# Optimization experiments

Measured on AMD Instinct MI355X. Metric: run time of the kernel, lower is better.

The kernel has to match this reference:

```python
import jax, jax.numpy as jnp
import numpy as np

ALPHA = 0.2  # LeakyReLU negative slope
NEG_BIG = jnp.float32(-9e15)


def _leaky_relu(x):
    return jnp.where(x > 0, x, ALPHA * x)


def gat_layer(h, adj, w, a):
    """One GATLayer with concat=True (ELU output), dropout=0 (eval mode).
    h: [N, F_in], adj: [N, N] int, w: [F_in, F_out], a: [2*F_out, 1].
    """
    Wh = h @ w                         # [N, F_out]
    f_out = w.shape[1]
    Wh1 = Wh @ a[:f_out]               # [N, 1]
    Wh2 = Wh @ a[f_out:]               # [N, 1]
    e = _leaky_relu(Wh1 + Wh2.T)       # [N, N] dense additive scores
    att = jnp.where(adj > 0, e, NEG_BIG)
    att = jax.nn.softmax(att, axis=1)  # row softmax
    return jax.nn.elu(att @ Wh)        # [N, F_out]


def setup_inputs() -> dict:
    N, F_IN, H, NHEADS = 4096, 128, 64, 4
    key = jax.random.key(0)
    ks = jax.random.split(key, 9)
    s = jnp.float32(0.1)  # keep logits in a sane range
    x = jax.random.normal(ks[0], (N, F_IN), jnp.float32)
    adj = jax.random.randint(ks[1], (N, N), 0, 2, jnp.int32)
    return {
        "x": x,
        "adj": adj,
        "w_heads": jax.random.normal(ks[2], (NHEADS, F_IN, H), jnp.float32) * s,
        "a_heads": jax.random.normal(ks[3], (NHEADS, 2 * H, 1), jnp.float32) * s,
        "w_out": jax.random.normal(ks[4], (NHEADS * H, H), jnp.float32) * s,
        "a_out": jax.random.normal(ks[5], (2 * H, 1), jnp.float32) * s,
        "lin_w": jax.random.normal(ks[6], (H, F_IN), jnp.float32) * s,
        "lin_b": jnp.zeros((H,), jnp.float32),
        "outlin_w": jax.random.normal(ks[7], (H, H), jnp.float32) * s,
        "outlin_b": jnp.zeros((H,), jnp.float32),
    }


def reference(x, adj, w_heads, a_heads, w_out, a_out, lin_w, lin_b, outlin_w, outlin_b):
    N = x.shape[0]
    x_residual = x @ lin_w.T + lin_b                      # nn.Linear(input, hidden)
    # multi-head GAT layers, concatenated along features
    heads = jax.vmap(gat_layer, in_axes=(None, None, 0, 0))(x, adj, w_heads, a_heads)  # [nh, N, H]
    hcat = jnp.transpose(heads, (1, 0, 2)).reshape(N, -1)  # [N, nh*H]
    out = gat_layer(hcat, adj, w_out, a_out)               # out_att (concat=True => ELU)
    out = (x_residual + out) @ outlin_w.T + outlin_b       # out_linear
    return jax.nn.elu(out)
```

## Files before the change

kernel.cpp:

```cpp
#include <hip/hip_runtime.h>
#include <hip/hip_bf16.h>
#include <stdint.h>

#define F_IN 128
#define H 64
#define NH 4
#define KCH_H 16
#define KCH_O 32
#define LOG2E 1.44269504088896f

typedef __attribute__((ext_vector_type(8))) short bf16x8;
typedef __attribute__((ext_vector_type(4))) float floatx4;

static __device__ __forceinline__ unsigned short f2bf(float v) {
    __hip_bfloat16 b = __float2bfloat16(v);
    return *(unsigned short*)&b;
}
static __device__ __forceinline__ float bf2f(unsigned short u) {
    return __uint_as_float((unsigned int)u << 16);
}

__global__ void prep_kernel(const int* __restrict__ adj,
                            unsigned char* __restrict__ adjp,
                            const float* __restrict__ x,
                            const float* __restrict__ w_heads,
                            const float* __restrict__ a_heads,
                            const float* __restrict__ lin_w,
                            const float* __restrict__ lin_b,
                            unsigned short* __restrict__ Bpk,
                            float* __restrict__ x_res,
                            float* __restrict__ s1h,
                            float* __restrict__ s2h, int N) {
    const int bid = blockIdx.x;
    const int tid = threadIdx.x;
    const int KT = N >> 5;
    const int WH_BLOCKS = N / 8;

    if (bid >= WH_BLOCKS) {
        int idx = bid - WH_BLOCKS;
        int it = idx >> 3, rem = idx & 7, half = rem >> 2, zz = rem & 3;
        int i0 = it * 16;
        int n = tid & 15, q = (tid >> 4) & 3, w = tid >> 6;
        const int* row = adj + (size_t)(i0 + n) * N;
        unsigned char* dst = adjp + (size_t)it * KT * 64;
        int ktbase = half * (KT / 2) + zz * 16 + w;
#pragma unroll
        for (int j = 0; j < 4; ++j) {
            int kt = ktbase + 4 * j;
            int c0 = kt * 32 + q * 8;
            int4 a = *(const int4*)(row + c0);
            int4 b = *(const int4*)(row + c0 + 4);
            unsigned byte =
                (unsigned)(a.x > 0) | ((unsigned)(a.y > 0) << 1) |
                ((unsigned)(a.z > 0) << 2) | ((unsigned)(a.w > 0) << 3) |
                ((unsigned)(b.x > 0) << 4) | ((unsigned)(b.y > 0) << 5) |
                ((unsigned)(b.z > 0) << 6) | ((unsigned)(b.w > 0) << 7);
            dst[kt * 64 + q * 16 + n] = (unsigned char)byte;
        }
        return;
    }

    int h = tid >> 6, f = tid & 63;
    int i0 = bid * 8;
    __shared__ float xs[8][F_IN];
    __shared__ float lwT[F_IN][65];
    for (int e = tid; e < 8 * F_IN; e += 256)
        xs[e >> 7][e & 127] = x[(size_t)(i0 + (e >> 7)) * F_IN + (e & 127)];
    for (int e = tid; e < 64 * F_IN; e += 256) {
        int ff = e >> 7, k = e & 127;
        lwT[k][ff] = lin_w[e];
    }
    __syncthreads();
    float acc[8];
#pragma unroll
    for (int r = 0; r < 8; ++r) acc[r] = 0.f;
    float xr0 = 0.f, xr1 = 0.f;
    const float* w = w_heads + (size_t)h * F_IN * H + f;
#pragma unroll 4
    for (int k = 0; k < F_IN; ++k) {
        float wv = w[(size_t)k * H];
#pragma unroll
        for (int r = 0; r < 8; ++r) acc[r] += xs[r][k] * wv;
        float wx = lwT[k][f];
        xr0 += xs[h][k] * wx;
        xr1 += xs[h + 4][k] * wx;
    }
    {
        int kt = i0 >> 5, qq = (i0 >> 3) & 3;
        union { unsigned short s[8]; uint4 v; } t;
#pragma unroll
        for (int r = 0; r < 8; ++r) t.s[r] = f2bf(acc[r]);
        unsigned short* d = Bpk +
            (((size_t)(h * KT + kt) * 4 + (f >> 4)) * 64 + qq * 16 + (f & 15)) * 8;
        *(uint4*)d = t.v;
    }
    float b = lin_b[f];
    x_res[(size_t)(i0 + h) * H + f] = xr0 + b;
    x_res[(size_t)(i0 + h + 4) * H + f] = xr1 + b;
    float a1v = a_heads[(size_t)h * 2 * H + f];
    float a2v = a_heads[(size_t)h * 2 * H + H + f];
#pragma unroll
    for (int r = 0; r < 8; ++r) {
        float t1 = acc[r] * a1v;
        float t2 = acc[r] * a2v;
#pragma unroll
        for (int off = 32; off > 0; off >>= 1) {
            t1 += __shfl_xor(t1, off, 64);
            t2 += __shfl_xor(t2, off, 64);
        }
        if (f == 0) {
            s1h[(size_t)h * N + i0 + r] = t1 * LOG2E;
            s2h[(size_t)h * N + i0 + r] = t2 * LOG2E;
        }
    }
}

template <int KTC>
__global__ __launch_bounds__(256, 8)
void pv2_kernel(const unsigned char* __restrict__ adjp,
                const unsigned short* __restrict__ Bpk,
                const float* __restrict__ s1a,
                const float* __restrict__ s2a,
                unsigned short* __restrict__ outp, float* __restrict__ lp,
                int out_stride, int N) {
    const int h = blockIdx.y, z = blockIdx.z;
    const int KT = N >> 5;
    const int kt0 = z * KTC;
    const int tid = threadIdx.x;
    const int wave = tid >> 6, lane = tid & 63;
    const int n = lane & 15, q = lane >> 4;
    const int i0w = (blockIdx.x * 4 + wave) * 16;

    __shared__ float s2s[KTC * 32];
    __shared__ unsigned short ldsB[2][2048];

    const float4* s2src = (const float4*)(s2a + (size_t)h * N + kt0 * 32);
    for (int e = tid; e < KTC * 8; e += 256) ((float4*)s2s)[e] = s2src[e];

    const unsigned short* Bb = Bpk + ((size_t)h * KT + kt0) * 2048;
    uint4 breg = *(const uint4*)(Bb + tid * 8);
    *(uint4*)&ldsB[0][tid * 8] = breg;
    breg = *(const uint4*)(Bb + 2048 + tid * 8);

    const unsigned char* ap = adjp + ((size_t)(i0w >> 4) * KT + kt0) * 64 + lane;
    unsigned int a_c = ap[0];
    unsigned int a_n = ap[64];
    const float s1v = s1a[(size_t)h * N + i0w + n];

    floatx4 acc[4];
    floatx4 accl = {0.f, 0.f, 0.f, 0.f};
#pragma unroll
    for (int g = 0; g < 4; ++g) acc[g] = (floatx4){0.f, 0.f, 0.f, 0.f};

    bf16x8 ones;
    {
        short one = (n == 0) ? (short)0x3F80 : (short)0;
#pragma unroll
        for (int jj = 0; jj < 8; ++jj) ones[jj] = one;
    }

    __syncthreads();

#pragma unroll 2
    for (int k = 0; k < KTC; ++k) {
        if (k + 1 < KTC) *(uint4*)&ldsB[(k + 1) & 1][tid * 8] = breg;
        unsigned int a_2 = 0;
        if (k + 2 < KTC) {
            breg = *(const uint4*)(Bb + (size_t)(k + 2) * 2048 + tid * 8);
            a_2 = ap[(size_t)(k + 2) * 64];
        }

        float4 sa = *(const float4*)&s2s[k * 32 + q * 8];
        float4 sb = *(const float4*)&s2s[k * 32 + q * 8 + 4];
        const float* sv = (const float*)&sa;
        const float* sw = (const float*)&sb;
        float e[8];
#pragma unroll
        for (int jj = 0; jj < 8; ++jj) {
            float sj = (jj < 4 ? sv[jj] : sw[jj - 4]);
            float tt = s1v + sj;
            float lr = fmaxf(tt, 0.2f * tt);
            lr = (a_c & (1u << jj)) ? lr : -150.f;
            e[jj] = __builtin_amdgcn_exp2f(lr);
        }
        union { unsigned int u[4]; bf16x8 v; } u;
        u.u[0] = __builtin_amdgcn_perm(__float_as_uint(e[1]), __float_as_uint(e[0]), 0x07060302u);
        u.u[1] = __builtin_amdgcn_perm(__float_as_uint(e[3]), __float_as_uint(e[2]), 0x07060302u);
        u.u[2] = __builtin_amdgcn_perm(__float_as_uint(e[5]), __float_as_uint(e[4]), 0x07060302u);
        u.u[3] = __builtin_amdgcn_perm(__float_as_uint(e[7]), __float_as_uint(e[6]), 0x07060302u);

        bf16x8 bf0 = *(const bf16x8*)&ldsB[k & 1][0 * 512 + lane * 8];
        bf16x8 bf1 = *(const bf16x8*)&ldsB[k & 1][1 * 512 + lane * 8];
        bf16x8 bf2 = *(const bf16x8*)&ldsB[k & 1][2 * 512 + lane * 8];
        bf16x8 bf3 = *(const bf16x8*)&ldsB[k & 1][3 * 512 + lane * 8];

        acc[0] = __builtin_amdgcn_mfma_f32_16x16x32_bf16(u.v, bf0, acc[0], 0, 0, 0);
        acc[1] = __builtin_amdgcn_mfma_f32_16x16x32_bf16(u.v, bf1, acc[1], 0, 0, 0);
        acc[2] = __builtin_amdgcn_mfma_f32_16x16x32_bf16(u.v, bf2, acc[2], 0, 0, 0);
        acc[3] = __builtin_amdgcn_mfma_f32_16x16x32_bf16(u.v, bf3, acc[3], 0, 0, 0);
        accl   = __builtin_amdgcn_mfma_f32_16x16x32_bf16(u.v, ones, accl, 0, 0, 0);

        a_c = a_n;
        a_n = a_2;
        __syncthreads();
    }

    unsigned short* obase = outp + ((size_t)z * N + i0w) * out_stride + h * 64;
#pragma unroll
    for (int r = 0; r < 4; ++r) {
        int rr = q * 4 + r;
        unsigned short* op = obase + (size_t)rr * out_stride + n;
        op[0]  = f2bf(acc[0][r]);
        op[16] = f2bf(acc[1][r]);
        op[32] = f2bf(acc[2][r]);
        op[48] = f2bf(acc[3][r]);
    }
    if (n == 0) {
        float* lrow = lp + ((size_t)z * gridDim.y + h) * N + i0w;
#pragma unroll
        for (int r = 0; r < 4; ++r) lrow[q * 4 + r] = accl[r];
    }
}

__global__ void whout2_kernel(const unsigned short* __restrict__ hcp,
                              const float* __restrict__ lhp,
                              const float* __restrict__ w_out,
                              const float* __restrict__ a_out,
                              unsigned short* __restrict__ BpkO,
                              float* __restrict__ s1o,
                              float* __restrict__ s2o, int N) {
    int tid = threadIdx.x;
    int i0 = blockIdx.x * 8;
    int KT = N >> 5;
    __shared__ float hs[8][256];
    __shared__ float linv[8][NH];
    if (tid < 8 * NH) {
        int r = tid >> 2, hd = tid & 3;
        float l = 0.f;
#pragma unroll
        for (int p = 0; p < KCH_H; ++p)
            l += lhp[((size_t)p * NH + hd) * N + i0 + r];
        linv[r][hd] = 1.f / fmaxf(l, 1e-30f);
    }
    __syncthreads();
    const size_t ps = (size_t)N * 256;
    for (int e = tid; e < 8 * 256; e += 256) {
        int r = e >> 8, k = e & 255;
        size_t off = (size_t)(i0 + r) * 256 + k;
        float v = 0.f;
#pragma unroll
        for (int p = 0; p < KCH_H; ++p) v += bf2f(hcp[p * ps + off]);
        v *= linv[r][k >> 6];
        hs[r][k] = v > 0.f ? v : expm1f(v);
    }
    __syncthreads();
    int f = tid & 63, rl = tid >> 6;
    float a0 = 0.f, a1 = 0.f;
#pragma unroll 4
    for (int k = 0; k < 256; ++k) {
        float wv = w_out[(size_t)k * H + f];
        a0 += hs[rl][k] * wv;
        a1 += hs[rl + 4][k] * wv;
    }
    float w1 = a_out[f], w2 = a_out[H + f];
    float t10 = a0 * w1, t20 = a0 * w2, t11 = a1 * w1, t21 = a1 * w2;
#pragma unroll
    for (int off = 32; off > 0; off >>= 1) {
        t10 += __shfl_xor(t10, off, 64);
        t20 += __shfl_xor(t20, off, 64);
        t11 += __shfl_xor(t11, off, 64);
        t21 += __shfl_xor(t21, off, 64);
    }
    if (f == 0) {
        s1o[i0 + rl] = t10 * LOG2E;
        s2o[i0 + rl] = t20 * LOG2E;
        s1o[i0 + rl + 4] = t11 * LOG2E;
        s2o[i0 + rl + 4] = t21 * LOG2E;
    }
    __syncthreads();
    float* wsW = &hs[0][0];
    wsW[rl * 64 + f] = a0;
    wsW[(rl + 4) * 64 + f] = a1;
    __syncthreads();
    if (tid < 64) {
        int kt = i0 >> 5, qq = (i0 >> 3) & 3;
        int g = tid >> 4, nn = tid & 15;
        union { unsigned short s[8]; uint4 v; } t;
#pragma unroll
        for (int r = 0; r < 8; ++r) t.s[r] = f2bf(wsW[r * 64 + g * 16 + nn]);
        unsigned short* d = BpkO +
            (((size_t)kt * 4 + g) * 64 + qq * 16 + nn) * 8;
        *(uint4*)d = t.v;
    }
}

__global__ void final2_kernel(const unsigned short* __restrict__ o2p,
                              const float* __restrict__ lop,
                              const float* __restrict__ x_res,
                              const float* __restrict__ outlin_w,
                              const float* __restrict__ outlin_b,
                              float* __restrict__ out, int N) {
    int tid = threadIdx.x;
    int f = tid & 63, rl = tid >> 6;
    int i0 = blockIdx.x * 8;
    __shared__ float hs[8][H];
    __shared__ float linv[8];
    if (tid < 8) {
        float l = 0.f;
#pragma unroll
        for (int p = 0; p < KCH_O; ++p) l += lop[(size_t)p * N + i0 + tid];
        linv[tid] = 1.f / fmaxf(l, 1e-30f);
    }
    __syncthreads();
    const size_t ps = (size_t)N * 64;
    for (int e = tid; e < 8 * 64; e += 256) {
        int r = e >> 6, ff = e & 63;
        size_t off = (size_t)(i0 + r) * 64 + ff;
        float v = 0.f;
#pragma unroll
        for (int p = 0; p < KCH_O; ++p) v += bf2f(o2p[p * ps + off]);
        v *= linv[r];
        v = v > 0.f ? v : expm1f(v);
        hs[r][ff] = v + x_res[off];
    }
    __syncthreads();
    float b = outlin_b[f];
    float a0 = b, a1 = b;
#pragma unroll 8
    for (int k = 0; k < H; ++k) {
        float wv = outlin_w[(size_t)f * H + k];
        a0 += hs[rl][k] * wv;
        a1 += hs[rl + 4][k] * wv;
    }
    a0 = a0 > 0.f ? a0 : expm1f(a0);
    a1 = a1 > 0.f ? a1 : expm1f(a1);
    out[(size_t)(i0 + rl) * H + f] = a0;
    out[(size_t)(i0 + rl + 4) * H + f] = a1;
}

extern "C" void kernel_launch(void* const* d_in, const int* in_sizes, int n_in,
                              void* d_out, int out_size, void* d_ws, size_t ws_size,
                              hipStream_t stream) {
    const float* x        = (const float*)d_in[0];
    const int*   adj      = (const int*)d_in[1];
    const float* w_heads  = (const float*)d_in[2];
    const float* a_heads  = (const float*)d_in[3];
    const float* w_out    = (const float*)d_in[4];
    const float* a_out    = (const float*)d_in[5];
    const float* lin_w    = (const float*)d_in[6];
    const float* lin_b    = (const float*)d_in[7];
    const float* outlin_w = (const float*)d_in[8];
    const float* outlin_b = (const float*)d_in[9];
    float* out = (float*)d_out;

    const int N = in_sizes[0] / F_IN;
    const int KT = N >> 5;

    char* p = (char*)d_ws;
    unsigned short* part = (unsigned short*)p;  p += (size_t)KCH_H * N * 256 * 2;
    float* x_res  = (float*)p;  p += (size_t)N * 64 * 4;
    float* s1h    = (float*)p;  p += (size_t)NH * N * 4;
    float* s2h    = (float*)p;  p += (size_t)NH * N * 4;
    float* s1o    = (float*)p;  p += (size_t)N * 4;
    float* s2o    = (float*)p;  p += (size_t)N * 4;
    float* lh_part = (float*)p; p += (size_t)KCH_H * NH * N * 4;
    float* lo_part = (float*)p; p += (size_t)KCH_O * N * 4;
    unsigned short* Bpk  = (unsigned short*)p;  p += (size_t)NH * KT * 2048 * 2;
    unsigned short* BpkO = (unsigned short*)p;  p += (size_t)KT * 2048 * 2;
    unsigned char* adjp  = (unsigned char*)p;   p += (size_t)(N / 16) * KT * 64;

    prep_kernel<<<N / 8 + (N / 16) * 8, 256, 0, stream>>>(
        adj, adjp, x, w_heads, a_heads, lin_w, lin_b, Bpk, x_res, s1h, s2h, N);
    pv2_kernel<8><<<dim3(N / 64, NH, KCH_H), 256, 0, stream>>>(
        adjp, Bpk, s1h, s2h, part, lh_part, NH * H, N);
    whout2_kernel<<<N / 8, 256, 0, stream>>>(part, lh_part, w_out, a_out,
                                             BpkO, s1o, s2o, N);
    pv2_kernel<4><<<dim3(N / 64, 1, KCH_O), 256, 0, stream>>>(
        adjp, BpkO, s1o, s2o, part, lo_part, H, N);
    final2_kernel<<<N / 8, 256, 0, stream>>>(part, lo_part, x_res, outlin_w, outlin_b, out, N);
}
```

Before: 195.9 us.

## Drop LDS staging in PV kernel, give each wave two row tiles

The attention-times-values kernel no longer stages B tiles through double-buffered shared memory with a per-iteration barrier. Each lane now loads its B fragments straight from global memory into registers, prefetched two steps ahead. The head layer's waves each cover two 16-row tiles so one set of B registers feeds twice as many MFMAs, and occupancy bounds are lowered to fit the extra registers. The reduction loops in whout2 and final2 now read partial sums as ushort4 vectors instead of scalars.

```diff
diff --git a/kernel.cpp b/kernel.cpp
--- a/kernel.cpp
+++ b/kernel.cpp
@@ -115,9 +115,9 @@
     }
 }
 
-template <int KTC>
-__global__ __launch_bounds__(256, 8)
-void pv2_kernel(const unsigned char* __restrict__ adjp,
+template <int KTC, int TILES>
+__global__ __launch_bounds__(256, 4)
+void pv4_kernel(const unsigned char* __restrict__ adjp,
                 const unsigned short* __restrict__ Bpk,
                 const float* __restrict__ s1a,
                 const float* __restrict__ s2a,
@@ -129,28 +129,41 @@
     const int tid = threadIdx.x;
     const int wave = tid >> 6, lane = tid & 63;
     const int n = lane & 15, q = lane >> 4;
-    const int i0w = (blockIdx.x * 4 + wave) * 16;
+    const int i0w = (blockIdx.x * 4 + wave) * (16 * TILES);
 
     __shared__ float s2s[KTC * 32];
-    __shared__ unsigned short ldsB[2][2048];
-
     const float4* s2src = (const float4*)(s2a + (size_t)h * N + kt0 * 32);
     for (int e = tid; e < KTC * 8; e += 256) ((float4*)s2s)[e] = s2src[e];
 
-    const unsigned short* Bb = Bpk + ((size_t)h * KT + kt0) * 2048;
-    uint4 breg = *(const uint4*)(Bb + tid * 8);
-    *(uint4*)&ldsB[0][tid * 8] = breg;
-    breg = *(const uint4*)(Bb + 2048 + tid * 8);
-
-    const unsigned char* ap = adjp + ((size_t)(i0w >> 4) * KT + kt0) * 64 + lane;
-    unsigned int a_c = ap[0];
-    unsigned int a_n = ap[64];
-    const float s1v = s1a[(size_t)h * N + i0w + n];
-
-    floatx4 acc[4];
-    floatx4 accl = {0.f, 0.f, 0.f, 0.f};
-#pragma unroll
-    for (int g = 0; g < 4; ++g) acc[g] = (floatx4){0.f, 0.f, 0.f, 0.f};
+    const unsigned short* Bb = Bpk + ((size_t)h * KT + kt0) * 2048 + lane * 8;
+
+    const unsigned char* arow[TILES];
+    float s1v[TILES];
+    unsigned int a_c[TILES], a_n[TILES];
+#pragma unroll
+    for (int t = 0; t < TILES; ++t) {
+        int rowgrp = (i0w >> 4) + t;
+        arow[t] = adjp + ((size_t)rowgrp * KT + kt0) * 64 + lane;
+        s1v[t] = s1a[(size_t)h * N + i0w + t * 16 + n];
+        a_c[t] = arow[t][0];
+        a_n[t] = arow[t][64];
+    }
+
+    bf16x8 bcur[4], bnxt[4];
+#pragma unroll
+    for (int g = 0; g < 4; ++g) {
+        bcur[g] = *(const bf16x8*)(Bb + g * 512);
+        bnxt[g] = *(const bf16x8*)(Bb + 2048 + g * 512);
+    }
+
+    floatx4 acc[TILES][4];
+    floatx4 accl[TILES];
+#pragma unroll
+    for (int t = 0; t < TILES; ++t) {
+        accl[t] = (floatx4){0.f, 0.f, 0.f, 0.f};
+#pragma unroll
+        for (int g = 0; g < 4; ++g) acc[t][g] = (floatx4){0.f, 0.f, 0.f, 0.f};
+    }
 
     bf16x8 ones;
     {
@@ -163,62 +176,74 @@
 
 #pragma unroll 2
     for (int k = 0; k < KTC; ++k) {
-        if (k + 1 < KTC) *(uint4*)&ldsB[(k + 1) & 1][tid * 8] = breg;
-        unsigned int a_2 = 0;
+        bf16x8 b2[4];
+        unsigned int a2[TILES];
         if (k + 2 < KTC) {
-            breg = *(const uint4*)(Bb + (size_t)(k + 2) * 2048 + tid * 8);
-            a_2 = ap[(size_t)(k + 2) * 64];
+#pragma unroll
+            for (int g = 0; g < 4; ++g)
+                b2[g] = *(const bf16x8*)(Bb + (size_t)(k + 2) * 2048 + g * 512);
+#pragma unroll
+            for (int t = 0; t < TILES; ++t) a2[t] = arow[t][(size_t)(k + 2) * 64];
         }
 
         float4 sa = *(const float4*)&s2s[k * 32 + q * 8];
         float4 sb = *(const float4*)&s2s[k * 32 + q * 8 + 4];
         const float* sv = (const float*)&sa;
         const float* sw = (const float*)&sb;
-        float e[8];
-#pragma unroll
-        for (int jj = 0; jj < 8; ++jj) {
-            float sj = (jj < 4 ? sv[jj] : sw[jj - 4]);
-            float tt = s1v + sj;
-            float lr = fmaxf(tt, 0.2f * tt);
-            lr = (a_c & (1u << jj)) ? lr : -150.f;
-            e[jj] = __builtin_amdgcn_exp2f(lr);
-        }
-        union { unsigned int u[4]; bf16x8 v; } u;
-        u.u[0] = __builtin_amdgcn_perm(__float_as_uint(e[1]), __float_as_uint(e[0]), 0x07060302u);
-        u.u[1] = __builtin_amdgcn_perm(__float_as_uint(e[3]), __float_as_uint(e[2]), 0x07060302u);
-        u.u[2] = __builtin_amdgcn_perm(__float_as_uint(e[5]), __float_as_uint(e[4]), 0x07060302u);
-        u.u[3] = __builtin_amdgcn_perm(__float_as_uint(e[7]), __float_as_uint(e[6]), 0x07060302u);
-
-        bf16x8 bf0 = *(const bf16x8*)&ldsB[k & 1][0 * 512 + lane * 8];
-        bf16x8 bf1 = *(const bf16x8*)&ldsB[k & 1][1 * 512 + lane * 8];
-        bf16x8 bf2 = *(const bf16x8*)&ldsB[k & 1][2 * 512 + lane * 8];
-        bf16x8 bf3 = *(const bf16x8*)&ldsB[k & 1][3 * 512 + lane * 8];
-
-        acc[0] = __builtin_amdgcn_mfma_f32_16x16x32_bf16(u.v, bf0, acc[0], 0, 0, 0);
-        acc[1] = __builtin_amdgcn_mfma_f32_16x16x32_bf16(u.v, bf1, acc[1], 0, 0, 0);
-        acc[2] = __builtin_amdgcn_mfma_f32_16x16x32_bf16(u.v, bf2, acc[2], 0, 0, 0);
-        acc[3] = __builtin_amdgcn_mfma_f32_16x16x32_bf16(u.v, bf3, acc[3], 0, 0, 0);
-        accl   = __builtin_amdgcn_mfma_f32_16x16x32_bf16(u.v, ones, accl, 0, 0, 0);
-
-        a_c = a_n;
-        a_n = a_2;
-        __syncthreads();
-    }
-
-    unsigned short* obase = outp + ((size_t)z * N + i0w) * out_stride + h * 64;
-#pragma unroll
-    for (int r = 0; r < 4; ++r) {
-        int rr = q * 4 + r;
-        unsigned short* op = obase + (size_t)rr * out_stride + n;
-        op[0]  = f2bf(acc[0][r]);
-        op[16] = f2bf(acc[1][r]);
-        op[32] = f2bf(acc[2][r]);
-        op[48] = f2bf(acc[3][r]);
-    }
-    if (n == 0) {
-        float* lrow = lp + ((size_t)z * gridDim.y + h) * N + i0w;
-#pragma unroll
-        for (int r = 0; r < 4; ++r) lrow[q * 4 + r] = accl[r];
+
+        bf16x8 af[TILES];
+#pragma unroll
+        for (int t = 0; t < TILES; ++t) {
+            float e[8];
+#pragma unroll
+            for (int jj = 0; jj < 8; ++jj) {
+                float sj = (jj < 4 ? sv[jj] : sw[jj - 4]);
+                float tt = s1v[t] + sj;
+                float lr = fmaxf(tt, 0.2f * tt);
+                lr = (a_c[t] & (1u << jj)) ? lr : -150.f;
+                e[jj] = __builtin_amdgcn_exp2f(lr);
+            }
+            union { unsigned int u[4]; bf16x8 v; } u;
+            u.u[0] = __builtin_amdgcn_perm(__float_as_uint(e[1]), __float_as_uint(e[0]), 0x07060302u);
+            u.u[1] = __builtin_amdgcn_perm(__float_as_uint(e[3]), __float_as_uint(e[2]), 0x07060302u);
+            u.u[2] = __builtin_amdgcn_perm(__float_as_uint(e[5]), __float_as_uint(e[4]), 0x07060302u);
+            u.u[3] = __builtin_amdgcn_perm(__float_as_uint(e[7]), __float_as_uint(e[6]), 0x07060302u);
+            af[t] = u.v;
+        }
+
+#pragma unroll
+        for (int g = 0; g < 4; ++g) {
+#pragma unroll
+            for (int t = 0; t < TILES; ++t)
+                acc[t][g] = __builtin_amdgcn_mfma_f32_16x16x32_bf16(af[t], bcur[g], acc[t][g], 0, 0, 0);
+        }
+#pragma unroll
+        for (int t = 0; t < TILES; ++t)
+            accl[t] = __builtin_amdgcn_mfma_f32_16x16x32_bf16(af[t], ones, accl[t], 0, 0, 0);
+
+#pragma unroll
+        for (int g = 0; g < 4; ++g) { bcur[g] = bnxt[g]; bnxt[g] = b2[g]; }
+#pragma unroll
+        for (int t = 0; t < TILES; ++t) { a_c[t] = a_n[t]; a_n[t] = a2[t]; }
+    }
+
+#pragma unroll
+    for (int t = 0; t < TILES; ++t) {
+        unsigned short* obase = outp + ((size_t)z * N + i0w + t * 16) * out_stride + h * 64;
+#pragma unroll
+        for (int r = 0; r < 4; ++r) {
+            int rr = q * 4 + r;
+            unsigned short* op = obase + (size_t)rr * out_stride + n;
+            op[0]  = f2bf(acc[t][0][r]);
+            op[16] = f2bf(acc[t][1][r]);
+            op[32] = f2bf(acc[t][2][r]);
+            op[48] = f2bf(acc[t][3][r]);
+        }
+        if (n == 0) {
+            float* lrow = lp + ((size_t)z * gridDim.y + h) * N + i0w + t * 16;
+#pragma unroll
+            for (int r = 0; r < 4; ++r) lrow[q * 4 + r] = accl[t][r];
+        }
     }
 }
 
@@ -244,14 +269,21 @@
     }
     __syncthreads();
     const size_t ps = (size_t)N * 256;
-    for (int e = tid; e < 8 * 256; e += 256) {
-        int r = e >> 8, k = e & 255;
-        size_t off = (size_t)(i0 + r) * 256 + k;
-        float v = 0.f;
-#pragma unroll
-        for (int p = 0; p < KCH_H; ++p) v += bf2f(hcp[p * ps + off]);
-        v *= linv[r][k >> 6];
-        hs[r][k] = v > 0.f ? v : expm1f(v);
+    for (int e4 = tid; e4 < 8 * 64; e4 += 256) {
+        int r = e4 >> 6, k4 = (e4 & 63) * 4;
+        size_t off = (size_t)(i0 + r) * 256 + k4;
+        float v0 = 0.f, v1 = 0.f, v2 = 0.f, v3 = 0.f;
+#pragma unroll
+        for (int p = 0; p < KCH_H; ++p) {
+            ushort4 u = *(const ushort4*)(hcp + p * ps + off);
+            v0 += bf2f(u.x); v1 += bf2f(u.y); v2 += bf2f(u.z); v3 += bf2f(u.w);
+        }
+        float li = linv[r][k4 >> 6];
+        v0 *= li; v1 *= li; v2 *= li; v3 *= li;
+        hs[r][k4]     = v0 > 0.f ? v0 : expm1f(v0);
+        hs[r][k4 + 1] = v1 > 0.f ? v1 : expm1f(v1);
+        hs[r][k4 + 2] = v2 > 0.f ? v2 : expm1f(v2);
+        hs[r][k4 + 3] = v3 > 0.f ? v3 : expm1f(v3);
     }
     __syncthreads();
     int f = tid & 63, rl = tid >> 6;
@@ -313,15 +345,26 @@
     }
     __syncthreads();
     const size_t ps = (size_t)N * 64;
-    for (int e = tid; e < 8 * 64; e += 256) {
-        int r = e >> 6, ff = e & 63;
-        size_t off = (size_t)(i0 + r) * 64 + ff;
-        float v = 0.f;
-#pragma unroll
-        for (int p = 0; p < KCH_O; ++p) v += bf2f(o2p[p * ps + off]);
-        v *= linv[r];
-        v = v > 0.f ? v : expm1f(v);
-        hs[r][ff] = v + x_res[off];
+    if (tid < 8 * 16) {
+        int r = tid >> 4, f4 = (tid & 15) * 4;
+        size_t off = (size_t)(i0 + r) * 64 + f4;
+        float v0 = 0.f, v1 = 0.f, v2 = 0.f, v3 = 0.f;
+#pragma unroll
+        for (int p = 0; p < KCH_O; ++p) {
+            ushort4 u = *(const ushort4*)(o2p + p * ps + off);
+            v0 += bf2f(u.x); v1 += bf2f(u.y); v2 += bf2f(u.z); v3 += bf2f(u.w);
+        }
+        float li = linv[r];
+        v0 *= li; v1 *= li; v2 *= li; v3 *= li;
+        v0 = v0 > 0.f ? v0 : expm1f(v0);
+        v1 = v1 > 0.f ? v1 : expm1f(v1);
+        v2 = v2 > 0.f ? v2 : expm1f(v2);
+        v3 = v3 > 0.f ? v3 : expm1f(v3);
+        const float* xr = x_res + off;
+        hs[r][f4]     = v0 + xr[0];
+        hs[r][f4 + 1] = v1 + xr[1];
+        hs[r][f4 + 2] = v2 + xr[2];
+        hs[r][f4 + 3] = v3 + xr[3];
     }
     __syncthreads();
     float b = outlin_b[f];
@@ -371,11 +414,11 @@
 
     prep_kernel<<<N / 8 + (N / 16) * 8, 256, 0, stream>>>(
         adj, adjp, x, w_heads, a_heads, lin_w, lin_b, Bpk, x_res, s1h, s2h, N);
-    pv2_kernel<8><<<dim3(N / 64, NH, KCH_H), 256, 0, stream>>>(
+    pv4_kernel<8, 2><<<dim3(N / 128, NH, KCH_H), 256, 0, stream>>>(
         adjp, Bpk, s1h, s2h, part, lh_part, NH * H, N);
     whout2_kernel<<<N / 8, 256, 0, stream>>>(part, lh_part, w_out, a_out,
                                              BpkO, s1o, s2o, N);
-    pv2_kernel<4><<<dim3(N / 64, 1, KCH_O), 256, 0, stream>>>(
+    pv4_kernel<4, 1><<<dim3(N / 64, 1, KCH_O), 256, 0, stream>>>(
         adjp, BpkO, s1o, s2o, part, lo_part, H, N);
     final2_kernel<<<N / 8, 256, 0, stream>>>(part, lo_part, x_res, outlin_w, outlin_b, out, N);
 }
```

After: 241.5 us. 1.23x slower.
